# Performance work log

Measured on AMD Instinct MI355X. Metric: run time of the kernel, lower is better.

## Reference

```python
import jax, jax.numpy as jnp
import numpy as np
from jax import lax

B, DIM, HEADS, H, W = 8, 64, 8, 256, 256
N_FFT = 128  # n in fft(); h//n == 2


def conv1x1(x, w):
    # x: [b,ci,h,w], w: [co,ci]
    return jnp.einsum('bchw,oc->bohw', x, w)


def conv2d(x, w, pad):
    # dense conv, w: [co,ci,kh,kw]
    return lax.conv_general_dilated(x, w, (1, 1), [(pad, pad), (pad, pad)],
                                    dimension_numbers=('NCHW', 'OIHW', 'NCHW'))


def dwconv3x3(x, w):
    # depthwise, w: [C,3,3]
    C = x.shape[1]
    return lax.conv_general_dilated(x, w[:, None], (1, 1), [(1, 1), (1, 1)],
                                    dimension_numbers=('NCHW', 'OIHW', 'NCHW'),
                                    feature_group_count=C)


def l2norm(t, eps=1e-12):
    n = jnp.sqrt(jnp.sum(t * t, axis=-1, keepdims=True))
    return t / jnp.maximum(n, eps)


def chanel_cross_attention(x, y, temp, qw, qdw, kvw, kvdw, projw):
    b, c, h, w = x.shape
    q = dwconv3x3(conv1x1(x, qw), qdw)          # [b,c,h,w]
    kv = dwconv3x3(conv1x1(y, kvw), kvdw)       # [b,2c,h,w]
    k, v = kv[:, :c], kv[:, c:]
    def rh(t):
        return t.reshape(b, HEADS, c // HEADS, h * w)
    q, k, v = rh(q), rh(k), rh(v)
    q = l2norm(q)
    k = l2norm(k)
    attn = jnp.einsum('bhcn,bhdn->bhcd', q, k) * temp  # temp [HEADS,1,1]
    attn = jax.nn.softmax(attn, axis=-1)
    out = jnp.einsum('bhcd,bhdn->bhcn', attn, v).reshape(b, c, h, w)
    return conv1x1(out, projw)


def fre_module_fft(x, conv1_w, rate_w1, rate_w2):
    x = conv2d(x, conv1_w, 1)                   # [B,DIM,H,W]
    h, w = x.shape[-2:]
    # dynamic threshold -> per-sample rectangular low-pass mask
    pooled = jnp.mean(x, axis=(2, 3))           # [B,DIM]
    t = jax.nn.gelu(pooled @ rate_w1.T, approximate=False) @ rate_w2.T
    thr = jax.nn.sigmoid(t)                     # [B,2]
    h_ = ((h // N_FFT) * thr[:, 0]).astype(jnp.int32)  # [B], trunc like .int()
    w_ = ((w // N_FFT) * thr[:, 1]).astype(jnp.int32)
    rows = jnp.arange(h)
    cols = jnp.arange(w)
    row_in = (rows[None, :] >= (h // 2 - h_)[:, None]) & (rows[None, :] < (h // 2 + h_)[:, None])
    col_in = (cols[None, :] >= (w // 2 - w_)[:, None]) & (cols[None, :] < (w // 2 + w_)[:, None])
    mask = (row_in[:, None, :, None] & col_in[:, None, None, :]).astype(x.dtype)  # [B,1,h,w]

    fft = jnp.fft.fft2(x, axes=(-2, -1), norm='forward')
    fft = jnp.roll(fft, (h // 2, w // 2), axis=(2, 3))        # shift
    def back(f):
        f = jnp.roll(f, (-(h // 2), -(w // 2)), axis=(2, 3))  # unshift
        return jnp.abs(jnp.fft.ifft2(f, axes=(-2, -1), norm='forward'))
    high = back(fft * (1.0 - mask))
    low = back(fft * mask)
    return high, low


def fre_refine(low, high, spatial_w, cg_w1, cg_w2, projw, projb):
    # SpatialGate(high)
    mx = jnp.max(high, axis=1, keepdims=True)
    mn = jnp.mean(high, axis=1, keepdims=True)
    sw = jax.nn.sigmoid(conv2d(jnp.concatenate([mx, mn], axis=1), spatial_w, 3))  # [b,1,h,w]
    # ChannelGate(low)
    def mlp(p):  # p: [b,dim]
        return (jax.nn.relu(p @ cg_w1.T) @ cg_w2.T)
    avg = mlp(jnp.mean(low, axis=(2, 3)))
    mxc = mlp(jnp.max(low, axis=(2, 3)))
    cw = jax.nn.sigmoid(avg + mxc)[:, :, None, None]  # [b,dim,1,1]
    out = low * sw + high * cw
    return conv1x1(out, projw) + projb[None, :, None, None]


def reference(x, y, conv1_w, rate_w1, rate_w2, cca_temp, cca_qw, cca_qdw,
              cca_kvw, cca_kvdw, cca_projw, spatial_w, cg_w1, cg_w2,
              refine_projw, refine_projb, para1, para2):
    b = y.shape[0]
    x = jax.image.resize(x, (b, x.shape[1], H, W), method='bilinear')
    high, low = fre_module_fft(x, conv1_w, rate_w1, rate_w2)
    def cca(i, a, bb):
        return chanel_cross_attention(a, bb, cca_temp[i], cca_qw[i], cca_qdw[i],
                                      cca_kvw[i], cca_kvdw[i], cca_projw[i])
    high = cca(0, high, y)   # channel_cross_l
    low = cca(1, low, y)     # channel_cross_h
    agg = fre_refine(low, high, spatial_w, cg_w1, cg_w2, refine_projw, refine_projb)
    out = cca(2, y, agg)     # channel_cross_agg
    return out * para1[None] + y * para2[None]


def setup_inputs() -> dict:
    key = jax.random.key(0)
    ks = jax.random.split(key, 18)
    def rn(k, shape, s=0.05):
        return jax.random.normal(k, shape, jnp.float32) * s
    return {
        'x': jax.random.normal(ks[0], (B, 3, 128, 128), jnp.float32),
        'y': jax.random.normal(ks[1], (B, DIM, H, W), jnp.float32),
        'conv1_w': rn(ks[2], (DIM, 3, 3, 3)),
        'rate_w1': rn(ks[3], (DIM // 8, DIM)),
        'rate_w2': rn(ks[4], (2, DIM // 8)),
        'cca_temp': jnp.ones((3, HEADS, 1, 1), jnp.float32),
        'cca_qw': rn(ks[5], (3, DIM, DIM)),
        'cca_qdw': rn(ks[6], (3, DIM, 3, 3)),
        'cca_kvw': rn(ks[7], (3, 2 * DIM, DIM)),
        'cca_kvdw': rn(ks[8], (3, 2 * DIM, 3, 3)),
        'cca_projw': rn(ks[9], (3, DIM, DIM)),
        'spatial_w': rn(ks[10], (1, 2, 7, 7)),
        'cg_w1': rn(ks[11], (DIM // 16, DIM)),
        'cg_w2': rn(ks[12], (DIM, DIM // 16)),
        'refine_projw': rn(ks[13], (DIM, DIM)),
        'refine_projb': rn(ks[14], (DIM,)),
        'para1': rn(ks[15], (DIM, 1, 1), 0.1),
        'para2': jnp.ones((DIM, 1, 1), jnp.float32),
    }
```

## Files before the change

kernel.cpp:

```cpp
#include <hip/hip_runtime.h>
#include <math.h>

#define HW_ 65536
#define NCHUNK 16
typedef long long i64;
#define TWO_PI 6.283185307179586476925f

typedef __bf16 bf16x8 __attribute__((ext_vector_type(8)));
typedef __bf16 bf16x4 __attribute__((ext_vector_type(4)));
typedef float f32x4 __attribute__((ext_vector_type(4)));

#define MFMA16(A,B,C) __builtin_amdgcn_mfma_f32_16x16x32_bf16(A,B,C,0,0,0)

__device__ __forceinline__ float sigm(float x){ return 1.0f/(1.0f+expf(-x)); }

__device__ __forceinline__ bf16x8 cvt_w8(const float* wp){
  float4 w0 = *(const float4*)wp;
  float4 w1 = *(const float4*)(wp+4);
  bf16x8 r;
  r[0]=(__bf16)w0.x; r[1]=(__bf16)w0.y; r[2]=(__bf16)w0.z; r[3]=(__bf16)w0.w;
  r[4]=(__bf16)w1.x; r[5]=(__bf16)w1.y; r[6]=(__bf16)w1.z; r[7]=(__bf16)w1.w;
  return r;
}

__device__ __forceinline__ void st_bf4(__bf16* p, float a, float b, float c, float d){
  bf16x4 v; v[0]=(__bf16)a; v[1]=(__bf16)b; v[2]=(__bf16)c; v[3]=(__bf16)d;
  *(bf16x4*)p = v;
}

__global__ __launch_bounds__(256) void k_resize(const float* __restrict__ x, float* __restrict__ R, int b0){
  int idx = blockIdx.x*256 + threadIdx.x;
  int ox = idx & 255;
  int oy = (idx >> 8) & 255;
  int bc = idx >> 16;
  int lb = bc/3; int c = bc - lb*3;
  float sx = ox*0.5f - 0.25f;
  float sy = oy*0.5f - 0.25f;
  int x0 = (int)floorf(sx); float fx = sx - (float)x0;
  int y0 = (int)floorf(sy); float fy = sy - (float)y0;
  int x1 = min(x0+1,127); int y1 = min(y0+1,127);
  x0 = max(x0,0); y0 = max(y0,0);
  const float* p = x + ((i64)(b0+lb)*3 + c)*16384;
  float v00=p[y0*128+x0], v01=p[y0*128+x1], v10=p[y1*128+x0], v11=p[y1*128+x1];
  R[idx] = (1.0f-fy)*((1.0f-fx)*v00 + fx*v01) + fy*((1.0f-fx)*v10 + fx*v11);
}

__global__ __launch_bounds__(256) void k_conv3(const float* __restrict__ R, const float* __restrict__ w, __bf16* __restrict__ out){
  int y = blockIdx.x & 255; int b = blockIdx.x >> 8; int t = threadIdx.x;
  float win[27];
  #pragma unroll
  for (int ci=0;ci<3;ci++){
    #pragma unroll
    for (int ky=0;ky<3;ky++){
      int yy = y+ky-1;
      const float* ip = R + (((i64)(b*3+ci))<<16) + yy*256;
      #pragma unroll
      for (int kx=0;kx<3;kx++){
        int xx = t+kx-1;
        float v = 0.f;
        if ((unsigned)yy<256u && (unsigned)xx<256u) v = ip[xx];
        win[ci*9+ky*3+kx] = v;
      }
    }
  }
  i64 obase = ((i64)b<<22) + (y<<8) + t;
  for (int o=0;o<64;o++){
    const float* wp = w + o*27;
    float acc=0.f;
    #pragma unroll
    for (int j=0;j<27;j++) acc += wp[j]*win[j];
    out[obase + ((i64)o<<16)] = (__bf16)acc;
  }
}

__global__ __launch_bounds__(256) void k_dft(const __bf16* __restrict__ xc, float* __restrict__ coeff, float* __restrict__ pooled){
  __shared__ float tc[256], ts[256];
  __shared__ float red[256];
  int t = threadIdx.x;
  float ang = TWO_PI * ((float)t/256.0f);
  tc[t] = cosf(ang); ts[t] = sinf(ang);
  __syncthreads();
  int bc = blockIdx.x;
  const __bf16* p = xc + (i64)bc*HW_;
  float s=0, cr=0, ci=0, rr=0, ri=0, dr=0, di=0;
  for (int i=t; i<HW_; i+=256){
    float v = (float)p[i];
    int col = i & 255, row = i >> 8, ds = (row+col)&255;
    s  += v;
    cr += v*tc[col]; ci += v*ts[col];
    rr += v*tc[row]; ri += v*ts[row];
    dr += v*tc[ds];  di += v*ts[ds];
  }
  float vals[7] = {s,cr,ci,rr,ri,dr,di};
  for (int j=0;j<7;j++){
    red[t] = vals[j]; __syncthreads();
    for (int st=128; st>0; st>>=1){ if (t<st) red[t]+=red[t+st]; __syncthreads(); }
    if (t==0) vals[j] = red[0];
    __syncthreads();
  }
  if (t==0){
    const float sc = 1.0f/65536.0f;
    for (int j=0;j<7;j++) coeff[bc*8+j] = vals[j]*sc;
    pooled[bc] = vals[0]*sc;
  }
}

__global__ __launch_bounds__(64) void k_thr(const float* __restrict__ pooled, const float* __restrict__ w1,
                      const float* __restrict__ w2, float* __restrict__ flag){
  __shared__ float hid[8];
  int b = blockIdx.x; int t = threadIdx.x;
  if (t < 8){
    float a = 0.f;
    for (int c=0;c<64;c++) a += pooled[b*64+c]*w1[t*64+c];
    hid[t] = 0.5f*a*(1.0f+erff(a*0.70710678118654752440f));
  }
  __syncthreads();
  if (t==0){
    float t0=0,t1=0;
    for (int k=0;k<8;k++){ t0 += hid[k]*w2[k]; t1 += hid[k]*w2[8+k]; }
    int h_ = (int)(2.0f*sigm(t0));
    int w_ = (int)(2.0f*sigm(t1));
    flag[b] = (h_>0 && w_>0) ? 1.0f : 0.0f;
  }
}

#define MM_SETUP \
  int t = threadIdx.x; \
  int lane = t & 63, wvi = t >> 6; \
  i64 px0 = (i64)blockIdx.x*256 + wvi*64; \
  int b = (int)(px0 >> 16); \
  int p0 = (int)(px0 & (HW_-1)); \
  i64 ibase = ((i64)b<<22) + p0; \
  int lm = lane & 15, kg = lane >> 4;

#define X8_SETUP_BLK(BLK) \
  int t = threadIdx.x; \
  int lane = t & 63, wvi = t >> 6; \
  i64 px0 = (i64)(BLK)*512 + (i64)wvi*128; \
  int b = (int)(px0 >> 16); \
  int p0 = (int)(px0 & (HW_-1)); \
  i64 ibase = ((i64)b<<22) + p0; \
  int lm = lane & 15, kg = lane >> 4;

#define X8_SETUP X8_SETUP_BLK(blockIdx.x)

#define X8_FILL_F32(in_ptr) \
  _Pragma("unroll") \
  for (int s=0;s<2;s++){ \
    _Pragma("unroll") \
    for (int j=0;j<8;j++){ \
      const float* p_ = (in_ptr) + ((i64)(s*32 + kg*8 + j)<<16) + 8*lm; \
      float4 a_ = *(const float4*)p_; \
      float4 c_ = *(const float4*)(p_+4); \
      bf[s][0][j]=(__bf16)a_.x; bf[s][1][j]=(__bf16)a_.y; bf[s][2][j]=(__bf16)a_.z; bf[s][3][j]=(__bf16)a_.w; \
      bf[s][4][j]=(__bf16)c_.x; bf[s][5][j]=(__bf16)c_.y; bf[s][6][j]=(__bf16)c_.z; bf[s][7][j]=(__bf16)c_.w; \
    } \
  }

#define X8_FILL_BF(in_ptr) \
  _Pragma("unroll") \
  for (int s=0;s<2;s++){ \
    _Pragma("unroll") \
    for (int j=0;j<8;j++){ \
      bf16x8 u_ = *(const bf16x8*)((in_ptr) + ((i64)(s*32 + kg*8 + j)<<16) + 8*lm); \
      _Pragma("unroll") \
      for (int e=0;e<8;e++) bf[s][e][j] = u_[e]; \
    } \
  }

#define X8_ACC_M(Wbase, BF) \
  bf16x8 af0 = cvt_w8((Wbase) + (m*16 + lm)*64 + kg*8); \
  bf16x8 af1 = cvt_w8((Wbase) + (m*16 + lm)*64 + 32 + kg*8); \
  f32x4 acc[8]; \
  _Pragma("unroll") \
  for (int e=0;e<8;e++){ f32x4 z_ = {0.f,0.f,0.f,0.f}; acc[e]=z_; } \
  _Pragma("unroll") \
  for (int e=0;e<8;e++){ acc[e]=MFMA16(af0,BF[0][e],acc[e]); acc[e]=MFMA16(af1,BF[1][e],acc[e]); }

#define X8_ST_BF(outp) \
  _Pragma("unroll") \
  for (int r=0;r<4;r++){ \
    int oc = m*16 + kg*4 + r; \
    bf16x8 ov; \
    _Pragma("unroll") \
    for (int e=0;e<8;e++) ov[e]=(__bf16)acc[e][r]; \
    *(bf16x8*)((outp) + ibase + ((i64)oc<<16) + 8*lm) = ov; \
  }

#define X8_MM_BF(Wbase, BF, outp) \
  _Pragma("unroll") \
  for (int m=0;m<4;m++){ X8_ACC_M(Wbase, BF) X8_ST_BF(outp) }

__global__ __launch_bounds__(256) void k_convq2(const __bf16* __restrict__ xc, const float* __restrict__ coeff,
      const float* __restrict__ flag, const float* __restrict__ qwh, const float* __restrict__ qwl,
      __bf16* __restrict__ outh, __bf16* __restrict__ outl){
  __shared__ float tc[256], ts[256];
  {
    int tt = threadIdx.x;
    float ang = TWO_PI * ((float)tt/256.0f);
    tc[tt]=cosf(ang); ts[tt]=sinf(ang);
  }
  __syncthreads();
  MM_SETUP
  float fl = flag[b];
  int y = p0 >> 8;
  int xb = (p0 & 255) + 4*lm;
  bf16x8 bfh[2][4], bfl[2][4];
  {
    float crow = tc[y], srow = ts[y];
    float cx[4], sx[4], cd[4], sd[4];
    #pragma unroll
    for (int e=0;e<4;e++){
      int xx = xb + e;
      cx[e]=tc[xx]; sx[e]=ts[xx];
      int d = (xx + y) & 255;
      cd[e]=tc[d]; sd[e]=ts[d];
    }
    #pragma unroll
    for (int s=0;s<2;s++){
      #pragma unroll
      for (int j=0;j<8;j++){
        int ch = s*32 + kg*8 + j;
        const float* cf = coeff + ((b<<6)+ch)*8;
        float4 ca = *(const float4*)cf;
        float4 cb = *(const float4*)(cf+4);
        float F00=ca.x, cR=ca.y, cI=ca.z, rR=ca.w, rI=cb.x, dR=cb.y, dI=cb.z;
        bf16x4 xr4 = *(const bf16x4*)(xc + ibase + ((i64)ch<<16) + 4*lm);
        float rowR = F00 + rR*crow + rI*srow;
        float rowI = rI*crow - rR*srow;
        #pragma unroll
        for (int e=0;e<4;e++){
          float re = rowR + cR*cx[e] + cI*sx[e] + dR*cd[e] + dI*sd[e];
          float im = rowI + cI*cx[e] - cR*sx[e] + dI*cd[e] - dR*sd[e];
          re*=fl; im*=fl;
          float vl = sqrtf(re*re+im*im);
          float hr = (float)xr4[e] - re;
          float vh = sqrtf(hr*hr + im*im);
          bfh[s][e][j] = (__bf16)vh;
          bfl[s][e][j] = (__bf16)vl;
        }
      }
    }
  }
  #pragma unroll
  for (int m=0;m<4;m++){
    bf16x8 af0 = cvt_w8(qwh + (m*16 + lm)*64 + kg*8);
    bf16x8 af1 = cvt_w8(qwh + (m*16 + lm)*64 + 32 + kg*8);
    f32x4 acc[4];
    #pragma unroll
    for (int e=0;e<4;e++){ f32x4 z={0.f,0.f,0.f,0.f}; acc[e]=z; }
    #pragma unroll
    for (int e=0;e<4;e++){ acc[e]=MFMA16(af0,bfh[0][e],acc[e]); acc[e]=MFMA16(af1,bfh[1][e],acc[e]); }
    #pragma unroll
    for (int r=0;r<4;r++){
      int oc = m*16 + kg*4 + r;
      st_bf4(outh + ibase + ((i64)oc<<16) + 4*lm, acc[0][r], acc[1][r], acc[2][r], acc[3][r]);
    }
  }
  #pragma unroll
  for (int m=0;m<4;m++){
    bf16x8 af0 = cvt_w8(qwl + (m*16 + lm)*64 + kg*8);
    bf16x8 af1 = cvt_w8(qwl + (m*16 + lm)*64 + 32 + kg*8);
    f32x4 acc[4];
    #pragma unroll
    for (int e=0;e<4;e++){ f32x4 z={0.f,0.f,0.f,0.f}; acc[e]=z; }
    #pragma unroll
    for (int e=0;e<4;e++){ acc[e]=MFMA16(af0,bfl[0][e],acc[e]); acc[e]=MFMA16(af1,bfl[1][e],acc[e]); }
    #pragma unroll
    for (int r=0;r<4;r++){
      int oc = m*16 + kg*4 + r;
      st_bf4(outl + ibase + ((i64)oc<<16) + 4*lm, acc[0][r], acc[1][r], acc[2][r], acc[3][r]);
    }
  }
}

__global__ __launch_bounds__(256) void k_kvq(const float* __restrict__ yin,
      const float* __restrict__ kvw0, const float* __restrict__ kvw1, const float* __restrict__ qw2,
      __bf16* __restrict__ k0o, __bf16* __restrict__ v0o,
      __bf16* __restrict__ k1o, __bf16* __restrict__ v1o, __bf16* __restrict__ q2o){
  X8_SETUP
  bf16x8 bf[2][8];
  X8_FILL_F32(yin + ibase)
  X8_MM_BF(kvw0,        bf, k0o)
  X8_MM_BF(kvw0 + 4096, bf, v0o)
  X8_MM_BF(kvw1,        bf, k1o)
  X8_MM_BF(kvw1 + 4096, bf, v1o)
  X8_MM_BF(qw2,         bf, q2o)
}

__global__ __launch_bounds__(256) void k_comb_kvb(const __bf16* __restrict__ lo2, const __bf16* __restrict__ hi2,
        const float* __restrict__ swb, const float* __restrict__ cwv,
        const float* __restrict__ w, const float* __restrict__ bias,
        const float* __restrict__ wkv,
        __bf16* __restrict__ kout, __bf16* __restrict__ vout){
  __shared__ __bf16 aggl[64][514];
  X8_SETUP
  int pxl = wvi*128 + 8*lm;
  const float* swp = swb + ((i64)b<<16) + p0 + 8*lm;
  float4 sw0 = *(const float4*)swp;
  float4 sw1 = *(const float4*)(swp+4);
  float swv[8] = {sw0.x,sw0.y,sw0.z,sw0.w,sw1.x,sw1.y,sw1.z,sw1.w};
  bf16x8 bf[2][8];
  #pragma unroll
  for (int s=0;s<2;s++){
    #pragma unroll
    for (int j=0;j<8;j++){
      int ch = s*32 + kg*8 + j;
      bf16x8 l8 = *(const bf16x8*)(lo2 + ibase + ((i64)ch<<16) + 8*lm);
      bf16x8 h8 = *(const bf16x8*)(hi2 + ibase + ((i64)ch<<16) + 8*lm);
      float cw = cwv[(b<<6) + ch];
      #pragma unroll
      for (int e=0;e<8;e++) bf[s][e][j] = (__bf16)((float)l8[e]*swv[e] + (float)h8[e]*cw);
    }
  }
  #pragma unroll
  for (int m=0;m<4;m++){
    X8_ACC_M(w, bf)
    #pragma unroll
    for (int r=0;r<4;r++){
      int oc = m*16 + kg*4 + r;
      float bv = bias[oc];
      bf16x8 ov;
      #pragma unroll
      for (int e=0;e<8;e++) ov[e]=(__bf16)(acc[e][r]+bv);
      *(bf16x8*)(&aggl[oc][pxl]) = ov;
    }
  }
  __syncthreads();
  bf16x8 bf2[2][8];
  #pragma unroll
  for (int s=0;s<2;s++){
    #pragma unroll
    for (int j=0;j<8;j++){
      int ch = s*32 + kg*8 + j;
      bf16x8 u_ = *(const bf16x8*)(&aggl[ch][pxl]);
      #pragma unroll
      for (int e=0;e<8;e++) bf2[s][e][j] = u_[e];
    }
  }
  X8_MM_BF(wkv,        bf2, kout)
  X8_MM_BF(wkv + 4096, bf2, vout)
}

__global__ __launch_bounds__(256) void k_mm_hilo(const __bf16* __restrict__ va, const __bf16* __restrict__ vb,
        const float* __restrict__ M0, const float* __restrict__ M1,
        float* __restrict__ mx, float* __restrict__ mn,
        __bf16* __restrict__ outa, __bf16* __restrict__ outb,
        float* __restrict__ spart, int hgrid){
  __shared__ float ls[4][64], lmx[4][64];
  int bx = blockIdx.x;
  int set = (bx >= hgrid) ? 1 : 0;
  int blk = bx - set*hgrid;
  X8_SETUP_BLK(blk)
  if (set == 0){
    bf16x8 bf[2][8];
    X8_FILL_BF(va + ibase)
    const float* Wb = M0 + ((i64)b<<12);
    float smx[8], ssum[8];
    #pragma unroll
    for (int e=0;e<8;e++){ smx[e]=-1e30f; ssum[e]=0.f; }
    #pragma unroll
    for (int m=0;m<4;m++){
      X8_ACC_M(Wb, bf)
      X8_ST_BF(outa)
      #pragma unroll
      for (int r=0;r<4;r++){
        #pragma unroll
        for (int e=0;e<8;e++){ smx[e]=fmaxf(smx[e],acc[e][r]); ssum[e]+=acc[e][r]; }
      }
    }
    #pragma unroll
    for (int e=0;e<8;e++){
      smx[e] = fmaxf(smx[e], __shfl_xor(smx[e],16));
      smx[e] = fmaxf(smx[e], __shfl_xor(smx[e],32));
      ssum[e] += __shfl_xor(ssum[e],16);
      ssum[e] += __shfl_xor(ssum[e],32);
    }
    if (kg==0){
      i64 pbase = ((i64)b<<16) + p0 + 8*lm;
      *(float4*)(mx+pbase)   = make_float4(smx[0],smx[1],smx[2],smx[3]);
      *(float4*)(mx+pbase+4) = make_float4(smx[4],smx[5],smx[6],smx[7]);
      const float iv = 1.0f/64.0f;
      *(float4*)(mn+pbase)   = make_float4(ssum[0]*iv,ssum[1]*iv,ssum[2]*iv,ssum[3]*iv);
      *(float4*)(mn+pbase+4) = make_float4(ssum[4]*iv,ssum[5]*iv,ssum[6]*iv,ssum[7]*iv);
    }
  } else {
    bf16x8 bf[2][8];
    X8_FILL_BF(vb + ibase)
    const float* Wb = M1 + ((i64)b<<12);
    #pragma unroll
    for (int m=0;m<4;m++){
      X8_ACC_M(Wb, bf)
      X8_ST_BF(outb)
      #pragma unroll
      for (int r=0;r<4;r++){
        int oc = m*16 + kg*4 + r;
        float s = 0.f, mm = -1e30f;
        #pragma unroll
        for (int e=0;e<8;e++){ s += acc[e][r]; mm = fmaxf(mm, acc[e][r]); }
        #pragma unroll
        for (int off=8; off; off>>=1){ s += __shfl_xor(s,off); mm = fmaxf(mm,__shfl_xor(mm,off)); }
        if (lm==0){ ls[wvi][oc]=s; lmx[wvi][oc]=mm; }
      }
    }
    __syncthreads();
    if (t<64){
      float s = ls[0][t]+ls[1][t]+ls[2][t]+ls[3][t];
      float mm = fmaxf(fmaxf(lmx[0][t],lmx[1][t]),fmaxf(lmx[2][t],lmx[3][t]));
      spart[(i64)blk*128 + t*2]   = s;
      spart[(i64)blk*128 + t*2+1] = mm;
    }
  }
}

__global__ __launch_bounds__(256) void k_mm_fin(const __bf16* __restrict__ v, const float* __restrict__ M,
      const float* __restrict__ para1, const float* __restrict__ para2,
      const float* __restrict__ yin, float* __restrict__ out){
  X8_SETUP
  bf16x8 bf[2][8];
  X8_FILL_BF(v + ibase)
  const float* Wb = M + ((i64)b<<12);
  #pragma unroll
  for (int m=0;m<4;m++){
    X8_ACC_M(Wb, bf)
    #pragma unroll
    for (int r=0;r<4;r++){
      int oc = m*16 + kg*4 + r;
      float p1 = para1[oc], p2 = para2[oc];
      const float* yp = yin + ibase + ((i64)oc<<16) + 8*lm;
      float4 y0 = *(const float4*)yp;
      float4 y1 = *(const float4*)(yp+4);
      float* op = out + ibase + ((i64)oc<<16) + 8*lm;
      *(float4*)op     = make_float4(acc[0][r]*p1+y0.x*p2, acc[1][r]*p1+y0.y*p2,
                                     acc[2][r]*p1+y0.z*p2, acc[3][r]*p1+y0.w*p2);
      *(float4*)(op+4) = make_float4(acc[4][r]*p1+y1.x*p2, acc[5][r]*p1+y1.y*p2,
                                     acc[6][r]*p1+y1.z*p2, acc[7][r]*p1+y1.w*p2);
    }
  }
}

__global__ __launch_bounds__(256) void k_gram(const __bf16* __restrict__ q0, const __bf16* __restrict__ kk0,
        const __bf16* __restrict__ q1, const __bf16* __restrict__ kk1,
        const float* __restrict__ qdw0, const float* __restrict__ kdw0,
        const float* __restrict__ qdw1, const float* __restrict__ kdw1,
        float* __restrict__ part, int hgrid){
  __shared__ __bf16 lds[2][2][16][264];
  __shared__ float red[4][16][16];
  int bx = blockIdx.x;
  int set = (bx >= hgrid) ? 1 : 0;
  int blk = bx - set*hgrid;
  const __bf16* qpre = set ? q1 : q0;
  const __bf16* kpre = set ? kk1 : kk0;
  const float* qdw = set ? qdw1 : qdw0;
  const float* kdw = set ? kdw1 : kdw0;
  float* ppart = part + (i64)set*hgrid*80;
  int rowblk = blk & 15;
  int bh = blk >> 4;
  int h = bh & 7, b = bh >> 3;
  int t = threadIdx.x;
  int lane = t & 63, wvi = t >> 6;
  int lm = lane & 15, kg = lane >> 4;
  const float* wp = (lm < 8 ? qdw : kdw) + h*72 + (lm&7)*9;
  float w0=wp[0],w1=wp[1],w2=wp[2],w3=wp[3],w4=wp[4],w5=wp[5],w6=wp[6],w7=wp[7],w8=wp[8];
  int p = t >> 4, seg = t & 15;
  const __bf16* plbase = (p < 8 ? qpre : kpre) + (((i64)((b<<6)+(h<<3)+(p&7)))<<16);
  int R0 = rowblk*16;

  float h0c[2][8], h1c[2][8];
  #pragma unroll
  for (int cc=0;cc<2;cc++)
    #pragma unroll
    for (int e=0;e<8;e++){ h0c[cc][e]=0.f; h1c[cc][e]=0.f; }
  f32x4 acc = {0.f,0.f,0.f,0.f};

  auto stage2 = [&](int bi, int ir){
    #pragma unroll
    for (int rr=0;rr<2;rr++){
      int r_ = ir + rr;
      __bf16* dst = &lds[bi][rr][p][seg*16];
      if ((unsigned)r_ < 256u){
        const __bf16* src = plbase + r_*256 + seg*16;
        bf16x8 a = *(const bf16x8*)src;
        bf16x8 c = *(const bf16x8*)(src+8);
        *(bf16x8*)dst = a; *(bf16x8*)(dst+8) = c;
      } else {
        bf16x8 z = {};
        *(bf16x8*)dst = z; *(bf16x8*)(dst+8) = z;
      }
    }
  };

  stage2(0, R0-1);
  __syncthreads();
  int buf = 0;
  for (int pr = 0; pr < 9; pr++){
    int irbase = R0-1 + 2*pr;
    if (pr < 8) stage2(buf^1, irbase+2);
    #pragma unroll
    for (int rr=0;rr<2;rr++){
      int ir = irbase + rr;
      const __bf16* rowp = &lds[buf][rr][lm][0];
      #pragma unroll
      for (int cc=0; cc<2; cc++){
        int xb = (wvi*2 + cc)*32 + kg*8;
        bf16x8 mid = *(const bf16x8*)(rowp + xb);
        float win[10];
        win[0] = (xb==0)   ? 0.f : (float)rowp[xb-1];
        #pragma unroll
        for (int w=1; w<9; w++) win[w] = (float)mid[w-1];
        win[9] = (xb==248) ? 0.f : (float)rowp[xb+8];
        float o[8];
        #pragma unroll
        for (int e=0;e<8;e++){
          float t0 = w0*win[e] + w1*win[e+1] + w2*win[e+2];
          float t1 = w3*win[e] + w4*win[e+1] + w5*win[e+2];
          float t2 = w6*win[e] + w7*win[e+1] + w8*win[e+2];
          o[e] = h0c[cc][e] + t2;
          h0c[cc][e] = h1c[cc][e] + t1;
          h1c[cc][e] = t0;
        }
        if (ir > R0){
          bf16x8 xf;
          #pragma unroll
          for (int e=0;e<8;e++) xf[e] = (__bf16)o[e];
          acc = MFMA16(xf, xf, acc);
        }
      }
    }
    __syncthreads();
    buf ^= 1;
  }
  #pragma unroll
  for (int r=0;r<4;r++) red[wvi][kg*4+r][lm] = acc[r];
  __syncthreads();
  if (t < 80){
    int r, c;
    if (t < 64){ r = t>>3; c = 8 + (t&7); }
    else if (t < 72){ r = t-64; c = r; }
    else { r = 8 + (t-72); c = r; }
    float s = red[0][r][c]+red[1][r][c]+red[2][r][c]+red[3][r][c];
    ppart[(i64)blk*80 + t] = s;
  }
}

__global__ __launch_bounds__(128) void k_stats_fin(const float* __restrict__ part, float* __restrict__ stats){
  int bh = blockIdx.x; int t = threadIdx.x;
  if (t < 80){
    float s=0.f;
    for (int c=0;c<NCHUNK;c++) s += part[((i64)bh*NCHUNK+c)*80 + t];
    stats[bh*80+t] = s;
  }
}

__global__ __launch_bounds__(64) void k_attn_m(const float* __restrict__ stats, const float* __restrict__ temp,
                         const float* __restrict__ projw, float* __restrict__ M, int nb){
  __shared__ float attn[8][8][8];
  int bsup = blockIdx.x; int t = threadIdx.x;
  int set = (bsup >= nb) ? 1 : 0;
  int h = t >> 3, cc = t & 7;
  const float* st = stats + (bsup*8+h)*80;
  float nq = fmaxf(sqrtf(st[64+cc]), 1e-12f);
  float tmp = temp[set*8 + h];
  const float* pw = projw + set*4096;
  float s[8];
  float mx = -1e30f;
  #pragma unroll
  for (int d=0;d<8;d++){
    float nk = fmaxf(sqrtf(st[72+d]), 1e-12f);
    s[d] = st[cc*8+d]/(nq*nk)*tmp;
    mx = fmaxf(mx, s[d]);
  }
  float sum=0.f;
  #pragma unroll
  for (int d=0;d<8;d++){ s[d]=expf(s[d]-mx); sum+=s[d]; }
  float inv = 1.0f/sum;
  #pragma unroll
  for (int d=0;d<8;d++) attn[h][cc][d] = s[d]*inv;
  __syncthreads();
  int o = t;
  for (int hh=0; hh<8; hh++){
    #pragma unroll
    for (int d=0; d<8; d++){
      float acc=0.f;
      #pragma unroll
      for (int c2=0;c2<8;c2++) acc += pw[o*64 + hh*8 + c2]*attn[hh][c2][d];
      M[((i64)bsup*64 + o)*64 + hh*8 + d] = acc;
    }
  }
}

__global__ __launch_bounds__(256) void k_dwb(const __bf16* __restrict__ in0, const __bf16* __restrict__ in1,
        const float* __restrict__ wd0, const float* __restrict__ wd1,
        __bf16* __restrict__ out0, __bf16* __restrict__ out1, int hgrid){
  int bx = blockIdx.x;
  int set = (bx >= hgrid) ? 1 : 0;
  int blk = bx - set*hgrid;
  const __bf16* in = set ? in1 : in0;
  const float* wd = set ? wd1 : wd0;
  __bf16* out = set ? out1 : out0;
  int half = blk & 1; int c = (blk>>1)&63; int b = blk>>7;
  int t = threadIdx.x;
  int strip = t & 31, rg = t >> 5;
  const __bf16* ip = in + (((i64)((b<<6)+c))<<16);
  __bf16* op = out + (((i64)((b<<6)+c))<<16);
  const float* wp = wd + c*9;
  float w0=wp[0],w1=wp[1],w2=wp[2],w3=wp[3],w4=wp[4],w5=wp[5],w6=wp[6],w7=wp[7],w8=wp[8];
  int R0 = half*128 + rg*16;
  int xb = strip*8;
  bool left = (xb==0), right = (xb==248);
  float h0[8], h1[8];
  #pragma unroll
  for (int e=0;e<8;e++){ h0[e]=0.f; h1[e]=0.f; }
  for (int ir = R0-1; ir <= R0+16; ir++){
    bool rok = ((unsigned)ir < 256u);
    float win[10];
    if (rok){
      const __bf16* rp = ip + ir*256 + xb;
      bf16x8 mid = *(const bf16x8*)rp;
      win[0] = left ? 0.f : (float)rp[-1];
      #pragma unroll
      for (int w=1; w<9; w++) win[w] = (float)mid[w-1];
      win[9] = right ? 0.f : (float)rp[8];
    } else {
      #pragma unroll
      for (int w=0; w<10; w++) win[w] = 0.f;
    }
    float o[8];
    #pragma unroll
    for (int e=0;e<8;e++){
      float t0 = w0*win[e] + w1*win[e+1] + w2*win[e+2];
      float t1 = w3*win[e] + w4*win[e+1] + w5*win[e+2];
      float t2 = w6*win[e] + w7*win[e+1] + w8*win[e+2];
      o[e] = h0[e] + t2;
      h0[e] = h1[e] + t1;
      h1[e] = t0;
    }
    if (ir > R0){
      bf16x8 ov;
      #pragma unroll
      for (int e=0;e<8;e++) ov[e] = (__bf16)o[e];
      *(bf16x8*)(op + (ir-1)*256 + xb) = ov;
    }
  }
}

__global__ __launch_bounds__(64) void k_spatcw(const float* __restrict__ spart,
                     const float* __restrict__ w1, const float* __restrict__ w2, float* __restrict__ cw){
  __shared__ float lm_[64], lx_[64];
  __shared__ float ha[4], hm[4];
  int b = blockIdx.x; int c = threadIdx.x;
  float s=0.f, m=-1e30f;
  for (int r=0;r<128;r++){
    s += spart[(i64)(b*128+r)*128 + c*2];
    m = fmaxf(m, spart[(i64)(b*128+r)*128 + c*2+1]);
  }
  lm_[c] = s*(1.0f/65536.0f);
  lx_[c] = m;
  __syncthreads();
  if (c < 4){
    float sa=0.f, sm_=0.f;
    for (int j=0;j<64;j++){ sa += w1[c*64+j]*lm_[j]; sm_ += w1[c*64+j]*lx_[j]; }
    ha[c] = fmaxf(sa, 0.f); hm[c] = fmaxf(sm_, 0.f);
  }
  __syncthreads();
  float a=0.f;
  #pragma unroll
  for (int j=0;j<4;j++) a += w2[c*4+j]*(ha[j]+hm[j]);
  cw[b*64+c] = sigm(a);
}

__global__ __launch_bounds__(256) void k_sw(const float* __restrict__ mx, const float* __restrict__ mn,
                     const float* __restrict__ w, float* __restrict__ sw){
  int row = blockIdx.x & 255; int b = blockIdx.x >> 8; int t = threadIdx.x;
  const float* m0 = mx + ((i64)b<<16);
  const float* m1 = mn + ((i64)b<<16);
  float acc=0.f;
  for (int ky=0;ky<7;ky++){
    int yy = row+ky-3; if ((unsigned)yy>255u) continue;
    for (int kx=0;kx<7;kx++){
      int xx = t+kx-3; if ((unsigned)xx>255u) continue;
      acc += w[ky*7+kx]*m0[yy*256+xx] + w[49+ky*7+kx]*m1[yy*256+xx];
    }
  }
  sw[((i64)b<<16) + row*256 + t] = sigm(acc);
}

extern "C" void kernel_launch(void* const* d_in, const int* in_sizes, int n_in,
                              void* d_out, int out_size, void* d_ws, size_t ws_size,
                              hipStream_t stream){
  const float* x      = (const float*)d_in[0];
  const float* y      = (const float*)d_in[1];
  const float* conv1w = (const float*)d_in[2];
  const float* ratew1 = (const float*)d_in[3];
  const float* ratew2 = (const float*)d_in[4];
  const float* temp   = (const float*)d_in[5];
  const float* qw     = (const float*)d_in[6];
  const float* qdw    = (const float*)d_in[7];
  const float* kvw    = (const float*)d_in[8];
  const float* kvdw   = (const float*)d_in[9];
  const float* projw  = (const float*)d_in[10];
  const float* spw    = (const float*)d_in[11];
  const float* cgw1   = (const float*)d_in[12];
  const float* cgw2   = (const float*)d_in[13];
  const float* rprojw = (const float*)d_in[14];
  const float* rprojb = (const float*)d_in[15];
  const float* para1  = (const float*)d_in[16];
  const float* para2  = (const float*)d_in[17];
  float* D = (float*)d_out;

  int nb = 8;
  for (;;){
    size_t unit = (size_t)nb*64*HW_;
    size_t pool = (size_t)nb*3*HW_
                + (size_t)nb*512 + (size_t)nb*64 + 64
                + 2*(size_t)nb*8*NCHUNK*80
                + 2*(size_t)nb*8*80
                + 2*(size_t)nb*64*64
                + 3*(size_t)nb*HW_
                + (size_t)nb*128*128
                + (size_t)nb*64;
    if ((3*unit + pool)*sizeof(float) <= ws_size || nb==1) break;
    nb >>= 1;
  }

  size_t unit = (size_t)nb*64*HW_;
  float* U0 = (float*)d_ws;
  float* U1 = U0 + unit;
  float* U2 = U1 + unit;
  float* sm = U2 + unit;
  float* Rbuf  = sm;  sm += (size_t)nb*3*HW_;
  float* coeff = sm;  sm += (size_t)nb*512;
  float* pooled= sm;  sm += (size_t)nb*64;
  float* flagb = sm;  sm += 64;
  float* part  = sm;  sm += 2*(size_t)nb*8*NCHUNK*80;
  float* stats = sm;  sm += 2*(size_t)nb*8*80;
  float* Mb    = sm;  sm += 2*(size_t)nb*64*64;
  float* mxmap = sm;  sm += (size_t)nb*HW_;
  float* mnmap = sm;  sm += (size_t)nb*HW_;
  float* swb   = sm;  sm += (size_t)nb*HW_;
  float* spart = sm;  sm += (size_t)nb*128*128;
  float* cwb   = sm;  sm += (size_t)nb*64;

  int hgr = nb*8*NCHUNK;
  int hdw = nb*128;
  int hmm = nb*128;

  for (int b0 = 0; b0 < 8; b0 += nb){
    const float* yg = y + (i64)b0*64*HW_;
    float*       Dg = D + (i64)b0*64*HW_;
    __bf16* U0a = (__bf16*)U0; __bf16* U0c = U0a + unit;
    __bf16* U1a = (__bf16*)U1; __bf16* U1c = U1a + unit;
    __bf16* U2a = (__bf16*)U2; __bf16* U2c = U2a + unit;
    __bf16* Dga = (__bf16*)Dg; __bf16* Dgc = Dga + unit;
    float* Mb1 = Mb + (i64)nb*4096;

    k_resize <<<nb*3*256, 256,0,stream>>>(x, Rbuf, b0);
    k_conv3  <<<nb*256,   256,0,stream>>>(Rbuf, conv1w, U0a);
    k_dft    <<<nb*64,    256,0,stream>>>(U0a, coeff, pooled);
    k_thr    <<<nb,       64, 0,stream>>>(pooled, ratew1, ratew2, flagb);

    k_convq2 <<<nb*256,256,0,stream>>>(U0a, coeff, flagb, qw + 0*4096, qw + 1*4096, U1a, U1c);
    k_kvq    <<<nb*128,256,0,stream>>>(yg, kvw + 0*8192, kvw + 1*8192, qw + 2*4096,
                                       U2a, Dga, U2c, Dgc, U0c);

    k_gram   <<<2*hgr,256,0,stream>>>(U1a, U2a, U1c, U2c,
                                      qdw + 0*576, kvdw + 0*1152, qdw + 1*576, kvdw + 1*1152,
                                      part, hgr);
    k_stats_fin<<<2*nb*8, 128,0,stream>>>(part, stats);
    k_dwb    <<<2*hdw,256,0,stream>>>(Dga, Dgc, kvdw + 0*1152 + 576, kvdw + 1*1152 + 576,
                                      U1a, U1c, hdw);
    k_attn_m <<<2*nb, 64,0,stream>>>(stats, temp, projw, Mb, nb);

    k_mm_hilo<<<2*hmm,256,0,stream>>>(U1a, U1c, Mb, Mb1, mxmap, mnmap, Dga, Dgc, spart, hmm);

    k_spatcw  <<<nb,     64, 0,stream>>>(spart, cgw1, cgw2, cwb);
    k_sw      <<<nb*256, 256,0,stream>>>(mxmap, mnmap, spw, swb);

    k_comb_kvb<<<nb*128,256,0,stream>>>(Dgc, Dga, swb, cwb, rprojw, rprojb,
                                        kvw + 2*8192, U2a, U2c);

    k_gram   <<<hgr,256,0,stream>>>(U0c, U2a, U0c, U2a,
                                    qdw + 2*576, kvdw + 2*1152, qdw + 2*576, kvdw + 2*1152,
                                    part, hgr);
    k_stats_fin<<<nb*8, 128,0,stream>>>(part, stats);
    k_dwb    <<<hdw,256,0,stream>>>(U2c, U2c, kvdw + 2*1152 + 576, kvdw + 2*1152 + 576,
                                    U1a, U1a, hdw);
    k_attn_m <<<nb, 64,0,stream>>>(stats, temp + 2*8, projw + 2*4096, Mb, nb);
    k_mm_fin <<<nb*128,256,0,stream>>>(U1a, Mb, para1, para2, yg, Dg);
  }
}
```

Baseline: 737.6 us.

## Fuse resize into conv3, spatial-weight conv into comb, stats reduction into attn

Removes three small kernels by folding their work into consumers: bilinear resize is recomputed inline inside the 3x3 conv, the 7x7 spatial-gate conv plus sigmoid is computed per block into shared memory inside k_comb_kvb, and the chunk-partial sum is done inside k_attn_m. This removes intermediate buffers (Rbuf, swb, stats) and several launches. In exchange, conv3 recomputes resize samples 9 times per pixel per channel, and the comb kernel adds a 98-tap stencil prologue before its MFMA work.

```diff
diff --git a/kernel.cpp b/kernel.cpp
--- a/kernel.cpp
+++ b/kernel.cpp
@@ -28,37 +28,32 @@
   *(bf16x4*)p = v;
 }
 
-__global__ __launch_bounds__(256) void k_resize(const float* __restrict__ x, float* __restrict__ R, int b0){
-  int idx = blockIdx.x*256 + threadIdx.x;
-  int ox = idx & 255;
-  int oy = (idx >> 8) & 255;
-  int bc = idx >> 16;
-  int lb = bc/3; int c = bc - lb*3;
-  float sx = ox*0.5f - 0.25f;
-  float sy = oy*0.5f - 0.25f;
+__device__ __forceinline__ float rsz(const float* p, int yy, int xx){
+  float sx = xx*0.5f - 0.25f;
+  float sy = yy*0.5f - 0.25f;
   int x0 = (int)floorf(sx); float fx = sx - (float)x0;
   int y0 = (int)floorf(sy); float fy = sy - (float)y0;
   int x1 = min(x0+1,127); int y1 = min(y0+1,127);
   x0 = max(x0,0); y0 = max(y0,0);
-  const float* p = x + ((i64)(b0+lb)*3 + c)*16384;
   float v00=p[y0*128+x0], v01=p[y0*128+x1], v10=p[y1*128+x0], v11=p[y1*128+x1];
-  R[idx] = (1.0f-fy)*((1.0f-fx)*v00 + fx*v01) + fy*((1.0f-fx)*v10 + fx*v11);
-}
-
-__global__ __launch_bounds__(256) void k_conv3(const float* __restrict__ R, const float* __restrict__ w, __bf16* __restrict__ out){
+  return (1.0f-fy)*((1.0f-fx)*v00 + fx*v01) + fy*((1.0f-fx)*v10 + fx*v11);
+}
+
+__global__ __launch_bounds__(256) void k_conv3r(const float* __restrict__ x, const float* __restrict__ w,
+                                                __bf16* __restrict__ out, int b0){
   int y = blockIdx.x & 255; int b = blockIdx.x >> 8; int t = threadIdx.x;
   float win[27];
   #pragma unroll
   for (int ci=0;ci<3;ci++){
+    const float* xp = x + ((i64)((b0+b)*3 + ci))*16384;
     #pragma unroll
     for (int ky=0;ky<3;ky++){
       int yy = y+ky-1;
-      const float* ip = R + (((i64)(b*3+ci))<<16) + yy*256;
       #pragma unroll
       for (int kx=0;kx<3;kx++){
         int xx = t+kx-1;
         float v = 0.f;
-        if ((unsigned)yy<256u && (unsigned)xx<256u) v = ip[xx];
+        if ((unsigned)yy<256u && (unsigned)xx<256u) v = rsz(xp, yy, xx);
         win[ci*9+ky*3+kx] = v;
       }
     }
@@ -289,17 +284,41 @@
 }
 
 __global__ __launch_bounds__(256) void k_comb_kvb(const __bf16* __restrict__ lo2, const __bf16* __restrict__ hi2,
-        const float* __restrict__ swb, const float* __restrict__ cwv,
+        const float* __restrict__ mxm, const float* __restrict__ mnm, const float* __restrict__ spw,
+        const float* __restrict__ cwv,
         const float* __restrict__ w, const float* __restrict__ bias,
         const float* __restrict__ wkv,
         __bf16* __restrict__ kout, __bf16* __restrict__ vout){
   __shared__ __bf16 aggl[64][514];
+  __shared__ float swl[512];
   X8_SETUP
   int pxl = wvi*128 + 8*lm;
-  const float* swp = swb + ((i64)b<<16) + p0 + 8*lm;
-  float4 sw0 = *(const float4*)swp;
-  float4 sw1 = *(const float4*)(swp+4);
-  float swv[8] = {sw0.x,sw0.y,sw0.z,sw0.w,sw1.x,sw1.y,sw1.z,sw1.w};
+  {
+    int base_row = p0 >> 8;
+    int blk_p0 = (int)(((i64)blockIdx.x*512) & (HW_-1));
+    base_row = blk_p0 >> 8;
+    const float* m0 = mxm + ((i64)b<<16);
+    const float* m1 = mnm + ((i64)b<<16);
+    #pragma unroll
+    for (int half=0; half<2; half++){
+      int q = t + half*256;
+      int row = base_row + (q >> 8);
+      int col = q & 255;
+      float acc=0.f;
+      for (int ky=0;ky<7;ky++){
+        int yy = row+ky-3; if ((unsigned)yy>255u) continue;
+        for (int kx=0;kx<7;kx++){
+          int xx = col+kx-3; if ((unsigned)xx>255u) continue;
+          acc += spw[ky*7+kx]*m0[yy*256+xx] + spw[49+ky*7+kx]*m1[yy*256+xx];
+        }
+      }
+      swl[q] = sigm(acc);
+    }
+  }
+  __syncthreads();
+  float swv[8];
+  #pragma unroll
+  for (int e=0;e<8;e++) swv[e] = swl[pxl+e];
   bf16x8 bf[2][8];
   #pragma unroll
   for (int s=0;s<2;s++){
@@ -543,22 +562,22 @@
   }
 }
 
-__global__ __launch_bounds__(128) void k_stats_fin(const float* __restrict__ part, float* __restrict__ stats){
-  int bh = blockIdx.x; int t = threadIdx.x;
-  if (t < 80){
-    float s=0.f;
-    for (int c=0;c<NCHUNK;c++) s += part[((i64)bh*NCHUNK+c)*80 + t];
-    stats[bh*80+t] = s;
-  }
-}
-
-__global__ __launch_bounds__(64) void k_attn_m(const float* __restrict__ stats, const float* __restrict__ temp,
+__global__ __launch_bounds__(64) void k_attn_m(const float* __restrict__ part, const float* __restrict__ temp,
                          const float* __restrict__ projw, float* __restrict__ M, int nb){
+  __shared__ float stl[8][80];
   __shared__ float attn[8][8][8];
   int bsup = blockIdx.x; int t = threadIdx.x;
   int set = (bsup >= nb) ? 1 : 0;
+  for (int v = t; v < 640; v += 64){
+    int hh = v/80, j = v - hh*80;
+    i64 bh = (i64)bsup*8 + hh;
+    float s=0.f;
+    for (int c=0;c<NCHUNK;c++) s += part[(bh*NCHUNK+c)*80 + j];
+    stl[hh][j] = s;
+  }
+  __syncthreads();
   int h = t >> 3, cc = t & 7;
-  const float* st = stats + (bsup*8+h)*80;
+  const float* st = stl[h];
   float nq = fmaxf(sqrtf(st[64+cc]), 1e-12f);
   float tmp = temp[set*8 + h];
   const float* pw = projw + set*4096;
@@ -667,22 +686,6 @@
   #pragma unroll
   for (int j=0;j<4;j++) a += w2[c*4+j]*(ha[j]+hm[j]);
   cw[b*64+c] = sigm(a);
-}
-
-__global__ __launch_bounds__(256) void k_sw(const float* __restrict__ mx, const float* __restrict__ mn,
-                     const float* __restrict__ w, float* __restrict__ sw){
-  int row = blockIdx.x & 255; int b = blockIdx.x >> 8; int t = threadIdx.x;
-  const float* m0 = mx + ((i64)b<<16);
-  const float* m1 = mn + ((i64)b<<16);
-  float acc=0.f;
-  for (int ky=0;ky<7;ky++){
-    int yy = row+ky-3; if ((unsigned)yy>255u) continue;
-    for (int kx=0;kx<7;kx++){
-      int xx = t+kx-3; if ((unsigned)xx>255u) continue;
-      acc += w[ky*7+kx]*m0[yy*256+xx] + w[49+ky*7+kx]*m1[yy*256+xx];
-    }
-  }
-  sw[((i64)b<<16) + row*256 + t] = sigm(acc);
 }
 
 extern "C" void kernel_launch(void* const* d_in, const int* in_sizes, int n_in,
@@ -711,12 +714,10 @@
   int nb = 8;
   for (;;){
     size_t unit = (size_t)nb*64*HW_;
-    size_t pool = (size_t)nb*3*HW_
-                + (size_t)nb*512 + (size_t)nb*64 + 64
+    size_t pool = (size_t)nb*512 + (size_t)nb*64 + 64
                 + 2*(size_t)nb*8*NCHUNK*80
-                + 2*(size_t)nb*8*80
                 + 2*(size_t)nb*64*64
-                + 3*(size_t)nb*HW_
+                + 2*(size_t)nb*HW_
                 + (size_t)nb*128*128
                 + (size_t)nb*64;
     if ((3*unit + pool)*sizeof(float) <= ws_size || nb==1) break;
@@ -728,16 +729,13 @@
   float* U1 = U0 + unit;
   float* U2 = U1 + unit;
   float* sm = U2 + unit;
-  float* Rbuf  = sm;  sm += (size_t)nb*3*HW_;
   float* coeff = sm;  sm += (size_t)nb*512;
   float* pooled= sm;  sm += (size_t)nb*64;
   float* flagb = sm;  sm += 64;
   float* part  = sm;  sm += 2*(size_t)nb*8*NCHUNK*80;
-  float* stats = sm;  sm += 2*(size_t)nb*8*80;
   float* Mb    = sm;  sm += 2*(size_t)nb*64*64;
   float* mxmap = sm;  sm += (size_t)nb*HW_;
   float* mnmap = sm;  sm += (size_t)nb*HW_;
-  float* swb   = sm;  sm += (size_t)nb*HW_;
   float* spart = sm;  sm += (size_t)nb*128*128;
   float* cwb   = sm;  sm += (size_t)nb*64;
 
@@ -754,8 +752,7 @@
     __bf16* Dga = (__bf16*)Dg; __bf16* Dgc = Dga + unit;
     float* Mb1 = Mb + (i64)nb*4096;
 
-    k_resize <<<nb*3*256, 256,0,stream>>>(x, Rbuf, b0);
-    k_conv3  <<<nb*256,   256,0,stream>>>(Rbuf, conv1w, U0a);
+    k_conv3r <<<nb*256,   256,0,stream>>>(x, conv1w, U0a, b0);
     k_dft    <<<nb*64,    256,0,stream>>>(U0a, coeff, pooled);
     k_thr    <<<nb,       64, 0,stream>>>(pooled, ratew1, ratew2, flagb);
 
@@ -766,26 +763,23 @@
     k_gram   <<<2*hgr,256,0,stream>>>(U1a, U2a, U1c, U2c,
                                       qdw + 0*576, kvdw + 0*1152, qdw + 1*576, kvdw + 1*1152,
                                       part, hgr);
-    k_stats_fin<<<2*nb*8, 128,0,stream>>>(part, stats);
     k_dwb    <<<2*hdw,256,0,stream>>>(Dga, Dgc, kvdw + 0*1152 + 576, kvdw + 1*1152 + 576,
                                       U1a, U1c, hdw);
-    k_attn_m <<<2*nb, 64,0,stream>>>(stats, temp, projw, Mb, nb);
+    k_attn_m <<<2*nb, 64,0,stream>>>(part, temp, projw, Mb, nb);
 
     k_mm_hilo<<<2*hmm,256,0,stream>>>(U1a, U1c, Mb, Mb1, mxmap, mnmap, Dga, Dgc, spart, hmm);
 
     k_spatcw  <<<nb,     64, 0,stream>>>(spart, cgw1, cgw2, cwb);
-    k_sw      <<<nb*256, 256,0,stream>>>(mxmap, mnmap, spw, swb);
-
-    k_comb_kvb<<<nb*128,256,0,stream>>>(Dgc, Dga, swb, cwb, rprojw, rprojb,
+
+    k_comb_kvb<<<nb*128,256,0,stream>>>(Dgc, Dga, mxmap, mnmap, spw, cwb, rprojw, rprojb,
                                         kvw + 2*8192, U2a, U2c);
 
     k_gram   <<<hgr,256,0,stream>>>(U0c, U2a, U0c, U2a,
                                     qdw + 2*576, kvdw + 2*1152, qdw + 2*576, kvdw + 2*1152,
                                     part, hgr);
-    k_stats_fin<<<nb*8, 128,0,stream>>>(part, stats);
     k_dwb    <<<hdw,256,0,stream>>>(U2c, U2c, kvdw + 2*1152 + 576, kvdw + 2*1152 + 576,
                                     U1a, U1a, hdw);
-    k_attn_m <<<nb, 64,0,stream>>>(stats, temp + 2*8, projw + 2*4096, Mb, nb);
+    k_attn_m <<<nb, 64,0,stream>>>(part, temp + 2*8, projw + 2*4096, Mb, nb);
     k_mm_fin <<<nb*128,256,0,stream>>>(U1a, Mb, para1, para2, yg, Dg);
   }
 }
```

New measurement: 767.9 us. +4.1%, slower.
